# Performance work log

Hardware: AMD Instinct MI355X
Metric: run time of the kernel (lower is better)

Reference implementation:

```python
import jax, jax.numpy as jnp
import numpy as np

B, S, D = 2, 2048, 2048
H, KV = 16, 4          # n_heads, n_kv_heads
HD = D // H            # head_dim = 128
FFN = 5632
EPS = 1e-6


def rmsnorm(t, w):
    return (t * jax.lax.rsqrt(jnp.mean(t * t, axis=-1, keepdims=True) + EPS)) * w


def setup_inputs() -> dict:
    key = jax.random.key(0)
    ks = jax.random.split(key, 12)
    # rotary tables: cos/sin stacked in last dim -> [S, HD//2, 2]
    inv_freq = 1.0 / (10000.0 ** (np.arange(0, HD, 2, dtype=np.float32) / HD))
    t = np.arange(S, dtype=np.float32)
    ang = np.einsum('s,f->sf', t, inv_freq)
    freqs_cis = jnp.asarray(np.stack([np.cos(ang), np.sin(ang)], axis=-1))
    p = lambda k, shape: jax.random.normal(k, shape, dtype=jnp.float32) * 0.02
    return {
        'x': jax.random.normal(ks[0], (B, S, D), dtype=jnp.float32),
        'velocity': jnp.zeros((B, S, D), dtype=jnp.float32),
        'freqs_cis': freqs_cis,
        'pre_norm_w': jnp.ones((D,), jnp.float32),
        'wq': p(ks[1], (D, H * HD)),
        'wk': p(ks[2], (D, KV * HD)),
        'wv': p(ks[3], (D, KV * HD)),
        'wo': p(ks[4], (H * HD, D)),
        'q_norm_w': jnp.ones((HD,), jnp.float32),
        'k_norm_w': jnp.ones((HD,), jnp.float32),
        'log_beta': jnp.float32(np.log(0.5 / 0.5)),  # sigmoid -> 0.5
        'ffn_norm_w': jnp.ones((D,), jnp.float32),
        'w1': p(ks[5], (D, FFN)),
        'w3': p(ks[6], (D, FFN)),
        'w2': p(ks[7], (FFN, D)),
    }


def _rope(t, cos, sin):
    # t: [B,S,h,HD]; cos/sin broadcast [1,S,1,HD//2]
    tr = t.reshape(*t.shape[:-1], HD // 2, 2)
    t0, t1 = tr[..., 0], tr[..., 1]
    return jnp.stack([t0 * cos - t1 * sin, t0 * sin + t1 * cos], axis=-1).reshape(t.shape)


def reference(x, velocity, freqs_cis, pre_norm_w, wq, wk, wv, wo,
              q_norm_w, k_norm_w, log_beta, ffn_norm_w, w1, w3, w2):
    h = rmsnorm(x, pre_norm_w)
    q = (h @ wq).reshape(B, S, H, HD)
    k = (h @ wk).reshape(B, S, KV, HD)
    v = (h @ wv).reshape(B, S, KV, HD)
    # qk-norm (per-head RMSNorm), then rotary
    q = rmsnorm(q, q_norm_w)
    k = rmsnorm(k, k_norm_w)
    cos = freqs_cis[None, :, None, :, 0]
    sin = freqs_cis[None, :, None, :, 1]
    q = _rope(q, cos, sin)
    k = _rope(k, cos, sin)
    # GQA: repeat kv heads
    k = jnp.repeat(k, H // KV, axis=2)
    v = jnp.repeat(v, H // KV, axis=2)
    scores = jnp.einsum('bqhd,bkhd->bhqk', q, k) / jnp.float32(np.sqrt(HD))
    # exclusive self-attention: attend strictly to past (j < i); row 0 -> zeros
    excl = jnp.tril(jnp.ones((S, S), bool), k=-1)
    probs = jax.nn.softmax(jnp.where(excl, scores, jnp.float32(-1e30)), axis=-1)
    probs = probs * excl  # exact zeros on masked cols; row 0 fully zero
    attn_out = jnp.einsum('bhqk,bkhd->bqhd', probs, v).reshape(B, S, D) @ wo
    # sigmoid-gated momentum residual with clamp
    beta = jax.nn.sigmoid(log_beta)
    velocity = jnp.clip(beta * velocity + attn_out, -8.0, 8.0)
    x = x + velocity
    # inlined RMSNorm recompute + SwiGLU FFN
    normed = rmsnorm(x, ffn_norm_w)
    ffn = (jax.nn.silu(normed @ w1) * (normed @ w3)) @ w2
    return (x + ffn, velocity)
```

## Files before the change

### kernel.cpp

```cpp
#include <hip/hip_runtime.h>
#include <cstdint>
#include <cstddef>

typedef __bf16 bf16;
typedef __bf16 bf16x2 __attribute__((ext_vector_type(2)));
typedef __bf16 bf16x8 __attribute__((ext_vector_type(8)));
typedef float  f32x4  __attribute__((ext_vector_type(4)));

#define DEV __device__ __forceinline__

constexpr int Bc = 2, Sc = 2048, Dc = 2048, Hc = 16, KVc = 4, HDc = 128, FFNc = 5632;
constexpr int Rc = Bc * Sc;

DEV void async16(const bf16* g, bf16* l) {
  __builtin_amdgcn_global_load_lds((const __attribute__((address_space(1))) void*)g,
                                   (__attribute__((address_space(3))) void*)l, 16, 0, 0);
}

__global__ void transpose_cast(const float* __restrict__ in, bf16* __restrict__ out,
                               int K, int N, int rowoff, int ldout) {
  __shared__ float tile[32][33];
  int k0 = blockIdx.y * 32, n0 = blockIdx.x * 32;
  int tx = threadIdx.x, ty = threadIdx.y;
  for (int r = ty; r < 32; r += 8)
    tile[r][tx] = in[(size_t)(k0 + r) * N + n0 + tx];
  __syncthreads();
  for (int r = ty; r < 32; r += 8)
    out[(size_t)(rowoff + n0 + r) * ldout + k0 + tx] = (bf16)tile[tx][r];
}

__global__ void transpose_v(const bf16* __restrict__ qkvb, bf16* __restrict__ vht) {
  __shared__ bf16 tile[32][33];
  int s0 = blockIdx.x * 32, d0 = blockIdx.y * 32, bg = blockIdx.z;
  int tx = threadIdx.x, ty = threadIdx.y;
  int b = bg >> 2, g = bg & 3;
  const bf16* src = qkvb + (size_t)(b * Sc) * 3072 + 2560 + g * 128;
  for (int r = ty; r < 32; r += 8)
    tile[r][tx] = src[(size_t)(s0 + r) * 3072 + d0 + tx];
  __syncthreads();
  bf16* dst = vht + ((size_t)bg * HDc) * Sc;
  for (int r = ty; r < 32; r += 8)
    dst[(size_t)(d0 + r) * Sc + s0 + tx] = tile[tx][r];
}

__global__ void rmsnorm_cast(const float* __restrict__ x, const float* __restrict__ w,
                             bf16* __restrict__ out) {
  __shared__ float red[4];
  int row = blockIdx.x, tid = threadIdx.x;
  const float* xr = x + (size_t)row * Dc;
  float ss = 0.f;
#pragma unroll
  for (int i = 0; i < Dc / 256; ++i) { float v = xr[tid + i * 256]; ss += v * v; }
  for (int off = 32; off; off >>= 1) ss += __shfl_xor(ss, off);
  if ((tid & 63) == 0) red[tid >> 6] = ss;
  __syncthreads();
  float rstd = rsqrtf((red[0] + red[1] + red[2] + red[3]) * (1.f / Dc) + 1e-6f);
  bf16* orow = out + (size_t)row * Dc;
#pragma unroll
  for (int i = 0; i < Dc / 256; ++i) {
    int j = tid + i * 256;
    orow[j] = (bf16)(xr[j] * rstd * w[j]);
  }
}

template <int MODE>
__global__ __launch_bounds__(256) void gemm_bt(
    const bf16* __restrict__ A, int lda, const bf16* __restrict__ Bt,
    float* __restrict__ Cf, bf16* __restrict__ Cb,
    const float* __restrict__ xin, const float* __restrict__ velin,
    const float* __restrict__ lbp, float* __restrict__ velout,
    int M, int N, int K, int ldc) {
  __shared__ bf16 As[2][128 * 32];
  __shared__ bf16 Bs[2][128 * 32];
  const int tid = threadIdx.x, lane = tid & 63, wvid = tid >> 6;
  const int quad = lane >> 4, l15 = lane & 15;
  const int m0 = blockIdx.y * 128, n0 = blockIdx.x * 128;
  const int wr = (wvid >> 1) * 64, wc = (wvid & 1) * 64;
  const int rsub = lane >> 2, chk = lane & 3;

  f32x4 acc[4][4];
  const f32x4 zf = {0.f, 0.f, 0.f, 0.f};
#pragma unroll
  for (int i = 0; i < 4; ++i)
#pragma unroll
    for (int j = 0; j < 4; ++j) acc[i][j] = zf;

  const bf16* Ag = A + (size_t)(m0 + wvid * 32 + rsub) * lda + chk * 8;
  const bf16* Bg = Bt + (size_t)(n0 + wvid * 32 + rsub) * K + chk * 8;
  const int lo = (wvid * 32) * 32;

  for (int k0 = 0; k0 < K; k0 += 64) {
#pragma unroll
    for (int hhalf = 0; hhalf < 2; ++hhalf) {
      int kk = k0 + hhalf * 32;
      async16(Ag + kk, As[hhalf] + lo);
      async16(Ag + (size_t)16 * lda + kk, As[hhalf] + lo + 16 * 32);
      async16(Bg + kk, Bs[hhalf] + lo);
      async16(Bg + (size_t)16 * K + kk, Bs[hhalf] + lo + 16 * 32);
    }
    __syncthreads();
#pragma unroll
    for (int hhalf = 0; hhalf < 2; ++hhalf) {
      bf16x8 af[4], bfr[4];
#pragma unroll
      for (int i = 0; i < 4; ++i)
        af[i] = *(const bf16x8*)(As[hhalf] + (wr + i * 16 + l15) * 32 + quad * 8);
#pragma unroll
      for (int j = 0; j < 4; ++j)
        bfr[j] = *(const bf16x8*)(Bs[hhalf] + (wc + j * 16 + l15) * 32 + quad * 8);
#pragma unroll
      for (int i = 0; i < 4; ++i)
#pragma unroll
        for (int j = 0; j < 4; ++j)
          acc[i][j] = __builtin_amdgcn_mfma_f32_16x16x32_bf16(af[i], bfr[j], acc[i][j], 0, 0, 0);
    }
    __syncthreads();
  }

  float beta = 0.f;
  if (MODE == 1) beta = 1.f / (1.f + __expf(-lbp[0]));
#pragma unroll
  for (int i = 0; i < 4; ++i) {
#pragma unroll
    for (int j = 0; j < 4; ++j) {
#pragma unroll
      for (int r = 0; r < 4; ++r) {
        int row = m0 + wr + i * 16 + quad * 4 + r;
        int col = n0 + wc + j * 16 + l15;
        size_t idx = (size_t)row * ldc + col;
        float c = acc[i][j][r];
        if (MODE == 1) {
          float v = beta * velin[idx] + c;
          v = fminf(8.f, fmaxf(-8.f, v));
          velout[idx] = v;
          Cf[idx] = xin[idx] + v;
        } else if (MODE == 2) {
          Cb[idx] = (bf16)c;
        } else {
          Cf[idx] = xin[idx] + c;
        }
      }
    }
  }
}

__global__ __launch_bounds__(256) void qk_norm_rope(
    const bf16* __restrict__ qkv, const float* __restrict__ qw, const float* __restrict__ kw,
    const float* __restrict__ freqs, bf16* __restrict__ qh, bf16* __restrict__ kh) {
  int row = blockIdx.x;
  int b = row >> 11, s = row & 2047;
  int tid = threadIdx.x, wvid = tid >> 6, lane = tid & 63;
  float cs = freqs[(size_t)(s * 64 + lane) * 2 + 0];
  float sn = freqs[(size_t)(s * 64 + lane) * 2 + 1];
  for (int slot = wvid; slot < 20; slot += 4) {
    const bf16* base = qkv + (size_t)row * 3072 + slot * 128;
    float t0 = (float)base[2 * lane], t1 = (float)base[2 * lane + 1];
    float ss = t0 * t0 + t1 * t1;
    for (int off = 32; off; off >>= 1) ss += __shfl_xor(ss, off);
    float rstd = rsqrtf(ss * (1.f / 128.f) + 1e-6f);
    const float* w = (slot < 16) ? qw : kw;
    float sc = (slot < 16) ? 0.08838834764831845f : 1.f;
    float n0 = t0 * rstd * w[2 * lane], n1 = t1 * rstd * w[2 * lane + 1];
    bf16x2 o;
    o[0] = (bf16)((n0 * cs - n1 * sn) * sc);
    o[1] = (bf16)((n0 * sn + n1 * cs) * sc);
    if (slot < 16)
      *(bf16x2*)(qh + ((size_t)(b * Hc + slot) * Sc + s) * HDc + 2 * lane) = o;
    else
      *(bf16x2*)(kh + ((size_t)(b * KVc + (slot - 16)) * Sc + s) * HDc + 2 * lane) = o;
  }
}

__global__ __launch_bounds__(256) void flash_attn(
    const bf16* __restrict__ qh, const bf16* __restrict__ kh, const bf16* __restrict__ vht,
    bf16* __restrict__ attn) {
  __shared__ bf16 Ks[2][64 * 128];
  __shared__ bf16 Vs[2][128 * 64];
  __shared__ bf16 Ps[4][16 * 68];
  const int tid = threadIdx.x, lane = tid & 63, wvid = tid >> 6;
  const int quad = lane >> 4, l15 = lane & 15;
  const int pairp = blockIdx.x;
  const int h = blockIdx.y, b = blockIdx.z, g = h >> 2;
  const bf16* qbase = qh + (size_t)(b * Hc + h) * Sc * HDc;
  const bf16* kbase = kh + (size_t)(b * KVc + g) * Sc * HDc;
  const bf16* vbase = vht + (size_t)(b * KVc + g) * HDc * Sc;
  const f32x4 zf = {0.f, 0.f, 0.f, 0.f};
  bf16* pw = Ps[wvid];

  bf16x8 ones;
#pragma unroll
  for (int e = 0; e < 8; ++e) ones[e] = (bf16)1.0f;

  int kcol[4], vcol[2];
#pragma unroll
  for (int f = 0; f < 4; ++f) kcol[f] = ((f * 64 + quad * 16) ^ (l15 << 4)) >> 1;
#pragma unroll
  for (int ks = 0; ks < 2; ++ks) vcol[ks] = ((ks * 64 + quad * 16) ^ ((l15 & 7) << 4)) >> 1;

  auto stage = [&](int kt2, int bsel) {
    const int k0s = kt2 * 64;
#pragma unroll
    for (int r = 0; r < 4; ++r) {
      int krow = (wvid * 4 + r) * 4 + quad;
      const bf16* src = kbase + (size_t)(k0s + krow) * HDc + ((l15 ^ (krow & 15)) * 8);
      async16(src, &Ks[bsel][(wvid * 4 + r) * 512]);
    }
#pragma unroll
    for (int r = 0; r < 4; ++r) {
      int vrow = (wvid * 4 + r) * 8 + (lane >> 3);
      int c8 = lane & 7;
      const bf16* src = vbase + (size_t)vrow * Sc + k0s + ((c8 ^ (vrow & 7)) * 8);
      async16(src, &Vs[bsel][(wvid * 4 + r) * 512]);
    }
  };

  for (int pass = 0; pass < 2; ++pass) {
    const int qt = pass ? 31 - pairp : pairp;
    const int q0 = qt * 64 + wvid * 16;

    bf16x8 qf[4];
#pragma unroll
    for (int f = 0; f < 4; ++f)
      qf[f] = *(const bf16x8*)(qbase + (size_t)(q0 + l15) * HDc + f * 32 + quad * 8);

    f32x4 Oa[8];
#pragma unroll
    for (int i = 0; i < 8; ++i) Oa[i] = zf;
    float m_i[4], l_i[4];
#pragma unroll
    for (int r = 0; r < 4; ++r) { m_i[r] = -3e38f; l_i[r] = 0.f; }

    const int ntiles = qt + 1;

    __syncthreads();
    stage(0, 0);

    for (int kt = 0; kt < ntiles; ++kt) {
      const int buf = kt & 1;
      const int k0 = kt * 64;
      __syncthreads();
      if (kt + 1 < ntiles) stage(kt + 1, buf ^ 1);

      f32x4 sc[4];
#pragma unroll
      for (int ks = 0; ks < 4; ++ks) {
        sc[ks] = zf;
#pragma unroll
        for (int f = 0; f < 4; ++f) {
          bf16x8 kf = *(const bf16x8*)(&Ks[buf][ks * 2048 + l15 * 128 + kcol[f]]);
          sc[ks] = __builtin_amdgcn_mfma_f32_16x16x32_bf16(qf[f], kf, sc[ks], 0, 0, 0);
        }
      }

      if (kt == qt) {
#pragma unroll
        for (int r = 0; r < 4; ++r) {
          int qg = q0 + quad * 4 + r;
#pragma unroll
          for (int ks = 0; ks < 4; ++ks)
            if (k0 + ks * 16 + l15 >= qg) sc[ks][r] = -3e38f;
        }
      }

      float mx[4], al[4];
#pragma unroll
      for (int r = 0; r < 4; ++r)
        mx[r] = fmaxf(fmaxf(sc[0][r], sc[1][r]), fmaxf(sc[2][r], sc[3][r]));
#pragma unroll
      for (int off = 8; off; off >>= 1)
#pragma unroll
        for (int r = 0; r < 4; ++r) mx[r] = fmaxf(mx[r], __shfl_xor(mx[r], off));
#pragma unroll
      for (int r = 0; r < 4; ++r) {
        float mn = fmaxf(m_i[r], mx[r]);
        al[r] = __expf(m_i[r] - mn);
        m_i[r] = mn;
#pragma unroll
        for (int ks = 0; ks < 4; ++ks) {
          float p = (sc[ks][r] > -1e37f) ? __expf(sc[ks][r] - mn) : 0.f;
          sc[ks][r] = p;
        }
      }

#pragma unroll
      for (int r = 0; r < 4; ++r)
#pragma unroll
        for (int ks = 0; ks < 4; ++ks)
          pw[(quad * 4 + r) * 68 + ks * 16 + l15] = (bf16)sc[ks][r];

#pragma unroll
      for (int i = 0; i < 8; ++i)
#pragma unroll
        for (int r = 0; r < 4; ++r) Oa[i][r] *= al[r];

      bf16x8 pf0 = *(const bf16x8*)(pw + l15 * 68 + quad * 8);
      bf16x8 pf1 = *(const bf16x8*)(pw + l15 * 68 + 32 + quad * 8);

      f32x4 ls = zf;
      ls = __builtin_amdgcn_mfma_f32_16x16x32_bf16(pf0, ones, ls, 0, 0, 0);
      ls = __builtin_amdgcn_mfma_f32_16x16x32_bf16(pf1, ones, ls, 0, 0, 0);

#pragma unroll
      for (int i = 0; i < 8; ++i) {
        bf16x8 vf0 = *(const bf16x8*)(&Vs[buf][(i * 16 + l15) * 64 + vcol[0]]);
        Oa[i] = __builtin_amdgcn_mfma_f32_16x16x32_bf16(pf0, vf0, Oa[i], 0, 0, 0);
        bf16x8 vf1 = *(const bf16x8*)(&Vs[buf][(i * 16 + l15) * 64 + vcol[1]]);
        Oa[i] = __builtin_amdgcn_mfma_f32_16x16x32_bf16(pf1, vf1, Oa[i], 0, 0, 0);
      }
#pragma unroll
      for (int r = 0; r < 4; ++r) l_i[r] = l_i[r] * al[r] + ls[r];
    }

#pragma unroll
    for (int r = 0; r < 4; ++r) {
      float inv = (l_i[r] > 0.f) ? 1.f / l_i[r] : 0.f;
      int qg = q0 + quad * 4 + r;
      bf16* orow = attn + (size_t)(b * Sc + qg) * Dc + h * HDc;
#pragma unroll
      for (int i = 0; i < 8; ++i) orow[i * 16 + l15] = (bf16)(Oa[i][r] * inv);
    }
  }
}

__global__ __launch_bounds__(256) void silu_mul_ip(bf16* __restrict__ g) {
  int row = blockIdx.y * 4 + (threadIdx.x >> 6);
  int j0 = (blockIdx.x * 64 + (threadIdx.x & 63)) * 8;
  bf16* p = g + (size_t)row * (2 * FFNc) + j0;
  const bf16x8 a = *(const bf16x8*)p;
  const bf16x8 bb = *(const bf16x8*)(p + FFNc);
  bf16x8 o;
#pragma unroll
  for (int e = 0; e < 8; ++e) {
    float xa = (float)a[e], xb = (float)bb[e];
    float s = xa / (1.f + __expf(-xa));
    o[e] = (bf16)(s * xb);
  }
  *(bf16x8*)p = o;
}

extern "C" void kernel_launch(void* const* d_in, const int* in_sizes, int n_in,
                              void* d_out, int out_size, void* d_ws, size_t ws_size,
                              hipStream_t stream) {
  (void)in_sizes; (void)n_in; (void)out_size; (void)ws_size;
  const float* x    = (const float*)d_in[0];
  const float* vel  = (const float*)d_in[1];
  const float* frq  = (const float*)d_in[2];
  const float* prew = (const float*)d_in[3];
  const float* wq   = (const float*)d_in[4];
  const float* wk   = (const float*)d_in[5];
  const float* wvw  = (const float*)d_in[6];
  const float* wo   = (const float*)d_in[7];
  const float* qnw  = (const float*)d_in[8];
  const float* knw  = (const float*)d_in[9];
  const float* lb   = (const float*)d_in[10];
  const float* ffnw = (const float*)d_in[11];
  const float* w1   = (const float*)d_in[12];
  const float* w3   = (const float*)d_in[13];
  const float* w2   = (const float*)d_in[14];

  float* out0 = (float*)d_out;
  float* out1 = out0 + (size_t)Rc * Dc;

  char* ws = (char*)d_ws;
  bf16* W  = (bf16*)ws;
  bf16* R1 = (bf16*)(ws + (size_t)23068672);
  bf16* G  = (bf16*)(ws + (size_t)23068672 + 16777216);
  bf16* hbuf   = R1;
  bf16* attn   = R1;
  bf16* normed = R1;
  bf16* qkvb   = G;
  bf16* qhb    = G + (size_t)4096 * 3072;
  bf16* khb    = qhb + (size_t)2 * 16 * 2048 * 128;
  bf16* vht    = khb + (size_t)2 * 4 * 2048 * 128;
  bf16* gbuf   = G;

  dim3 tb(32, 8);

  transpose_cast<<<dim3(64, 64), tb, 0, stream>>>(wq, W, 2048, 2048, 0, 2048);
  transpose_cast<<<dim3(16, 64), tb, 0, stream>>>(wk, W, 2048, 512, 2048, 2048);
  transpose_cast<<<dim3(16, 64), tb, 0, stream>>>(wvw, W, 2048, 512, 2560, 2048);
  rmsnorm_cast<<<Rc, 256, 0, stream>>>(x, prew, hbuf);
  gemm_bt<2><<<dim3(24, 32), 256, 0, stream>>>(hbuf, 2048, W, nullptr, qkvb, nullptr, nullptr,
                                               nullptr, nullptr, 4096, 3072, 2048, 3072);
  qk_norm_rope<<<Rc, 256, 0, stream>>>(qkvb, qnw, knw, frq, qhb, khb);
  transpose_v<<<dim3(64, 4, 8), tb, 0, stream>>>(qkvb, vht);

  flash_attn<<<dim3(16, Hc, Bc), 256, 0, stream>>>(qhb, khb, vht, attn);
  transpose_cast<<<dim3(64, 64), tb, 0, stream>>>(wo, W, 2048, 2048, 0, 2048);
  gemm_bt<1><<<dim3(16, 32), 256, 0, stream>>>(attn, 2048, W, out0, nullptr, x, vel, lb, out1,
                                               4096, 2048, 2048, 2048);

  rmsnorm_cast<<<Rc, 256, 0, stream>>>(out0, ffnw, normed);
  transpose_cast<<<dim3(176, 64), tb, 0, stream>>>(w1, W, 2048, 5632, 0, 2048);
  gemm_bt<2><<<dim3(44, 32), 256, 0, stream>>>(normed, 2048, W, nullptr, gbuf, nullptr, nullptr,
                                               nullptr, nullptr, 4096, 5632, 2048, 11264);
  transpose_cast<<<dim3(176, 64), tb, 0, stream>>>(w3, W, 2048, 5632, 0, 2048);
  gemm_bt<2><<<dim3(44, 32), 256, 0, stream>>>(normed, 2048, W, nullptr, gbuf + FFNc, nullptr,
                                               nullptr, nullptr, nullptr, 4096, 5632, 2048, 11264);
  silu_mul_ip<<<dim3(11, 1024), 256, 0, stream>>>(gbuf);
  transpose_cast<<<dim3(64, 176), tb, 0, stream>>>(w2, W, 5632, 2048, 0, 5632);
  gemm_bt<3><<<dim3(16, 32), 256, 0, stream>>>(gbuf, 11264, W, out0, nullptr, out0, nullptr,
                                               nullptr, nullptr, 4096, 2048, 5632, 2048);
}
```

Baseline: 908.0 us.

## Replace GEMM with 256-row tiled, triple-buffered, LDS-swizzled MFMA kernel

Replaces the 128x128 double-buffered GEMM with a 512-thread kernel that computes 256xBN tiles, where BN is 128 or 256. It keeps a three-stage ring of async global-to-LDS loads gated by explicit vmcnt waits, and uses an XOR swizzle on the LDS layout to avoid bank conflicts. It also remaps block ids so neighbouring tiles land on the same XCD. The aim is to hide memory latency, raise operand reuse per tile and improve L2 locality across all the projection and FFN GEMMs, at the cost of more registers and LDS per block and hand-tuned wait counts that are easy to get wrong.

```diff
diff --git a/kernel.cpp b/kernel.cpp
--- a/kernel.cpp
+++ b/kernel.cpp
@@ -63,70 +63,122 @@
   }
 }
 
-template <int MODE>
-__global__ __launch_bounds__(256) void gemm_bt(
+DEV int swzofs(int r, int quad) {
+  int pr = r >> 1;
+  int g = (((r & 1) << 2) | quad) ^ (pr & 7);
+  return pr * 64 + g * 8;
+}
+
+template <int MODE, int NF>
+__global__ __launch_bounds__(512, 2) void gemm256(
     const bf16* __restrict__ A, int lda, const bf16* __restrict__ Bt,
     float* __restrict__ Cf, bf16* __restrict__ Cb,
     const float* __restrict__ xin, const float* __restrict__ velin,
     const float* __restrict__ lbp, float* __restrict__ velout,
-    int M, int N, int K, int ldc) {
-  __shared__ bf16 As[2][128 * 32];
-  __shared__ bf16 Bs[2][128 * 32];
-  const int tid = threadIdx.x, lane = tid & 63, wvid = tid >> 6;
+    int K, int ldc, int nbx) {
+  constexpr int BN = NF * 64;
+  constexpr int BLD = 2 + BN / 128;
+  __shared__ bf16 Asb[3][256 * 32];
+  __shared__ bf16 Bsb[3][BN * 32];
+  const int tid = threadIdx.x, lane = tid & 63, w = tid >> 6;
   const int quad = lane >> 4, l15 = lane & 15;
-  const int m0 = blockIdx.y * 128, n0 = blockIdx.x * 128;
-  const int wr = (wvid >> 1) * 64, wc = (wvid & 1) * 64;
-  const int rsub = lane >> 2, chk = lane & 3;
-
-  f32x4 acc[4][4];
+  const int wm = w >> 2, wn = w & 3;
+
+  const int nwg = gridDim.x, bid = blockIdx.x;
+  const int qq = nwg >> 3, rr = nwg & 7, xcd = bid & 7, lid = bid >> 3;
+  const int swz = (xcd < rr ? xcd * (qq + 1) : rr * (qq + 1) + (xcd - rr) * qq) + lid;
+  const int m0 = (swz / nbx) * 256, n0 = (swz % nbx) * BN;
+
+  const int NT = K >> 5;
+
+  f32x4 acc[8][NF];
   const f32x4 zf = {0.f, 0.f, 0.f, 0.f};
 #pragma unroll
-  for (int i = 0; i < 4; ++i)
-#pragma unroll
-    for (int j = 0; j < 4; ++j) acc[i][j] = zf;
-
-  const bf16* Ag = A + (size_t)(m0 + wvid * 32 + rsub) * lda + chk * 8;
-  const bf16* Bg = Bt + (size_t)(n0 + wvid * 32 + rsub) * K + chk * 8;
-  const int lo = (wvid * 32) * 32;
-
-  for (int k0 = 0; k0 < K; k0 += 64) {
-#pragma unroll
-    for (int hhalf = 0; hhalf < 2; ++hhalf) {
-      int kk = k0 + hhalf * 32;
-      async16(Ag + kk, As[hhalf] + lo);
-      async16(Ag + (size_t)16 * lda + kk, As[hhalf] + lo + 16 * 32);
-      async16(Bg + kk, Bs[hhalf] + lo);
-      async16(Bg + (size_t)16 * K + kk, Bs[hhalf] + lo + 16 * 32);
-    }
-    __syncthreads();
-#pragma unroll
-    for (int hhalf = 0; hhalf < 2; ++hhalf) {
-      bf16x8 af[4], bfr[4];
-#pragma unroll
-      for (int i = 0; i < 4; ++i)
-        af[i] = *(const bf16x8*)(As[hhalf] + (wr + i * 16 + l15) * 32 + quad * 8);
-#pragma unroll
-      for (int j = 0; j < 4; ++j)
-        bfr[j] = *(const bf16x8*)(Bs[hhalf] + (wc + j * 16 + l15) * 32 + quad * 8);
-#pragma unroll
-      for (int i = 0; i < 4; ++i)
-#pragma unroll
-        for (int j = 0; j < 4; ++j)
-          acc[i][j] = __builtin_amdgcn_mfma_f32_16x16x32_bf16(af[i], bfr[j], acc[i][j], 0, 0, 0);
-    }
-    __syncthreads();
+  for (int i = 0; i < 8; ++i)
+#pragma unroll
+    for (int j = 0; j < NF; ++j) acc[i][j] = zf;
+
+  auto stage = [&](int kt, int ring) {
+    const int k0 = kt * 32;
+#pragma unroll
+    for (int i = 0; i < 2; ++i) {
+      int fi = w * 2 + i;
+      int pr = fi * 8 + (lane >> 3), g0 = (lane & 7) ^ (pr & 7);
+      int r = pr * 2 + (g0 >> 2), c8 = (g0 & 3) * 8;
+      async16(A + (size_t)(m0 + r) * lda + k0 + c8, Asb[ring] + fi * 512);
+    }
+#pragma unroll
+    for (int i = 0; i < BN / 128; ++i) {
+      int fi = w * (BN / 128) + i;
+      int pr = fi * 8 + (lane >> 3), g0 = (lane & 7) ^ (pr & 7);
+      int r = pr * 2 + (g0 >> 2), c8 = (g0 & 3) * 8;
+      async16(Bt + (size_t)(n0 + r) * K + k0 + c8, Bsb[ring] + fi * 512);
+    }
+  };
+
+  stage(0, 0);
+  stage(1, 1);
+  if constexpr (BLD == 4) asm volatile("s_waitcnt vmcnt(4)" ::: "memory");
+  else                    asm volatile("s_waitcnt vmcnt(3)" ::: "memory");
+  __builtin_amdgcn_s_barrier();
+
+  int r0 = 0;
+  for (int kt = 0; kt < NT; ++kt) {
+    int r2 = r0 + 2; if (r2 >= 3) r2 -= 3;
+    const bf16* Ak = Asb[r0];
+    const bf16* Bk = Bsb[r0];
+    if (kt + 2 < NT) stage(kt + 2, r2);
+
+    bf16x8 bfr[NF], af[4];
+#pragma unroll
+    for (int j = 0; j < NF; ++j)
+      bfr[j] = *(const bf16x8*)(Bk + swzofs(wn * (NF * 16) + j * 16 + l15, quad));
+#pragma unroll
+    for (int i = 0; i < 4; ++i)
+      af[i] = *(const bf16x8*)(Ak + swzofs(wm * 128 + i * 16 + l15, quad));
+    __builtin_amdgcn_s_barrier();
+    __builtin_amdgcn_s_setprio(1);
+#pragma unroll
+    for (int i = 0; i < 4; ++i)
+#pragma unroll
+      for (int j = 0; j < NF; ++j)
+        acc[i][j] = __builtin_amdgcn_mfma_f32_16x16x32_bf16(af[i], bfr[j], acc[i][j], 0, 0, 0);
+    __builtin_amdgcn_s_setprio(0);
+    __builtin_amdgcn_s_barrier();
+
+#pragma unroll
+    for (int i = 0; i < 4; ++i)
+      af[i] = *(const bf16x8*)(Ak + swzofs(wm * 128 + 64 + i * 16 + l15, quad));
+    __builtin_amdgcn_s_barrier();
+    __builtin_amdgcn_s_setprio(1);
+#pragma unroll
+    for (int i = 0; i < 4; ++i)
+#pragma unroll
+      for (int j = 0; j < NF; ++j)
+        acc[4 + i][j] = __builtin_amdgcn_mfma_f32_16x16x32_bf16(af[i], bfr[j], acc[4 + i][j], 0, 0, 0);
+    __builtin_amdgcn_s_setprio(0);
+
+    if (kt + 2 < NT) {
+      if constexpr (BLD == 4) asm volatile("s_waitcnt vmcnt(4)" ::: "memory");
+      else                    asm volatile("s_waitcnt vmcnt(3)" ::: "memory");
+    } else if (kt + 2 == NT) {
+      asm volatile("s_waitcnt vmcnt(0)" ::: "memory");
+    }
+    __builtin_amdgcn_sched_barrier(0);
+    __builtin_amdgcn_s_barrier();
+    r0 = (r0 == 2) ? 0 : r0 + 1;
   }
 
   float beta = 0.f;
   if (MODE == 1) beta = 1.f / (1.f + __expf(-lbp[0]));
 #pragma unroll
-  for (int i = 0; i < 4; ++i) {
-#pragma unroll
-    for (int j = 0; j < 4; ++j) {
+  for (int i = 0; i < 8; ++i) {
+#pragma unroll
+    for (int j = 0; j < NF; ++j) {
 #pragma unroll
       for (int r = 0; r < 4; ++r) {
-        int row = m0 + wr + i * 16 + quad * 4 + r;
-        int col = n0 + wc + j * 16 + l15;
+        int row = m0 + wm * 128 + i * 16 + quad * 4 + r;
+        int col = n0 + wn * (NF * 16) + j * 16 + l15;
         size_t idx = (size_t)row * ldc + col;
         float c = acc[i][j][r];
         if (MODE == 1) {
@@ -380,25 +432,25 @@
   transpose_cast<<<dim3(16, 64), tb, 0, stream>>>(wk, W, 2048, 512, 2048, 2048);
   transpose_cast<<<dim3(16, 64), tb, 0, stream>>>(wvw, W, 2048, 512, 2560, 2048);
   rmsnorm_cast<<<Rc, 256, 0, stream>>>(x, prew, hbuf);
-  gemm_bt<2><<<dim3(24, 32), 256, 0, stream>>>(hbuf, 2048, W, nullptr, qkvb, nullptr, nullptr,
-                                               nullptr, nullptr, 4096, 3072, 2048, 3072);
+  gemm256<2, 4><<<192, 512, 0, stream>>>(hbuf, 2048, W, nullptr, qkvb, nullptr, nullptr,
+                                         nullptr, nullptr, 2048, 3072, 12);
   qk_norm_rope<<<Rc, 256, 0, stream>>>(qkvb, qnw, knw, frq, qhb, khb);
   transpose_v<<<dim3(64, 4, 8), tb, 0, stream>>>(qkvb, vht);
 
   flash_attn<<<dim3(16, Hc, Bc), 256, 0, stream>>>(qhb, khb, vht, attn);
   transpose_cast<<<dim3(64, 64), tb, 0, stream>>>(wo, W, 2048, 2048, 0, 2048);
-  gemm_bt<1><<<dim3(16, 32), 256, 0, stream>>>(attn, 2048, W, out0, nullptr, x, vel, lb, out1,
-                                               4096, 2048, 2048, 2048);
+  gemm256<1, 2><<<256, 512, 0, stream>>>(attn, 2048, W, out0, nullptr, x, vel, lb, out1,
+                                         2048, 2048, 16);
 
   rmsnorm_cast<<<Rc, 256, 0, stream>>>(out0, ffnw, normed);
   transpose_cast<<<dim3(176, 64), tb, 0, stream>>>(w1, W, 2048, 5632, 0, 2048);
-  gemm_bt<2><<<dim3(44, 32), 256, 0, stream>>>(normed, 2048, W, nullptr, gbuf, nullptr, nullptr,
-                                               nullptr, nullptr, 4096, 5632, 2048, 11264);
+  gemm256<2, 2><<<704, 512, 0, stream>>>(normed, 2048, W, nullptr, gbuf, nullptr, nullptr,
+                                         nullptr, nullptr, 2048, 11264, 44);
   transpose_cast<<<dim3(176, 64), tb, 0, stream>>>(w3, W, 2048, 5632, 0, 2048);
-  gemm_bt<2><<<dim3(44, 32), 256, 0, stream>>>(normed, 2048, W, nullptr, gbuf + FFNc, nullptr,
-                                               nullptr, nullptr, nullptr, 4096, 5632, 2048, 11264);
+  gemm256<2, 2><<<704, 512, 0, stream>>>(normed, 2048, W, nullptr, gbuf + FFNc, nullptr,
+                                         nullptr, nullptr, nullptr, 2048, 11264, 44);
   silu_mul_ip<<<dim3(11, 1024), 256, 0, stream>>>(gbuf);
   transpose_cast<<<dim3(64, 176), tb, 0, stream>>>(w2, W, 5632, 2048, 0, 5632);
-  gemm_bt<3><<<dim3(16, 32), 256, 0, stream>>>(gbuf, 11264, W, out0, nullptr, out0, nullptr,
-                                               nullptr, nullptr, 4096, 2048, 5632, 2048);
-}
+  gemm256<3, 2><<<256, 512, 0, stream>>>(gbuf, 11264, W, out0, nullptr, out0, nullptr,
+                                         nullptr, nullptr, 5632, 2048, 16);
+}
```

After: 1.052 ms. 1.16x slower.
